# Optimization experiments

Hardware: AMD Instinct MI355X
Metric: run time of the kernel (lower is better)

The kernel has to match this reference:

```python
import jax, jax.numpy as jnp
import numpy as np

N_RAYS, N_SAMPLES = 8192, 128
RANK, RES = 32, 512


def setup_inputs() -> dict:
    key = jax.random.key(0)
    k0, k1, k2, k3 = jax.random.split(key, 4)
    pts = jax.random.uniform(k0, (N_RAYS, N_SAMPLES, 3), dtype=jnp.float32)
    # 3 plane grids for coord combos (0,1),(0,2),(1,2); torch shape [1,rank,H,W] -> [rank,H,W]
    grid_xy = jax.random.normal(k1, (RANK, RES, RES), dtype=jnp.float32) * 0.1
    grid_xz = jax.random.normal(k2, (RANK, RES, RES), dtype=jnp.float32) * 0.1
    grid_yz = jax.random.normal(k3, (RANK, RES, RES), dtype=jnp.float32) * 0.1
    aabb = jnp.array([[-1.0, -1.0, -1.0], [1.0, 1.0, 1.0]], dtype=jnp.float32)
    return {"pts": pts, "grid_xy": grid_xy, "grid_xz": grid_xz, "grid_yz": grid_yz, "aabb": aabb}


def _grid_sample2d(grid, coords):
    """Bilinear grid_sample, align_corners=True. grid [R,H,W], coords [N,2] in [-1,1] (x,y).
    Returns [N,R]."""
    H, W = grid.shape[1], grid.shape[2]
    x = (coords[:, 0] + 1.0) * 0.5 * (W - 1)
    y = (coords[:, 1] + 1.0) * 0.5 * (H - 1)
    x0 = jnp.floor(x)
    y0 = jnp.floor(y)
    wx = x - x0
    wy = y - y0
    x0i = jnp.clip(x0.astype(jnp.int32), 0, W - 1)
    x1i = jnp.clip(x0i + 1, 0, W - 1)
    y0i = jnp.clip(y0.astype(jnp.int32), 0, H - 1)
    y1i = jnp.clip(y0i + 1, 0, H - 1)
    v00 = grid[:, y0i, x0i]  # [R,N]
    v01 = grid[:, y0i, x1i]
    v10 = grid[:, y1i, x0i]
    v11 = grid[:, y1i, x1i]
    out = (v00 * (1 - wx) * (1 - wy) + v01 * wx * (1 - wy)
           + v10 * (1 - wx) * wy + v11 * wx * wy)
    return out.T  # [N,R]


def reference(pts, grid_xy, grid_xz, grid_yz, aabb):
    n_rays, n_samples, _ = pts.shape
    # normalize world coords to [-1,1]
    p = (pts - aabb[0]) * (2.0 / (aabb[1] - aabb[0])) - 1.0
    p = p.reshape(-1, 3)
    # multiply-reduce over the 3 coordinate-plane interpolations
    interp = (_grid_sample2d(grid_xy, p[:, (0, 1)])
              * _grid_sample2d(grid_xz, p[:, (0, 2)])
              * _grid_sample2d(grid_yz, p[:, (1, 2)]))  # [N, rank]
    density = jnp.mean(interp, axis=-1).reshape(n_rays, n_samples, 1)
    return jnp.exp(density)  # trunc_exp density activation
```

## Files before the change

kernel.cpp:

```cpp
#include <hip/hip_runtime.h>
#include <hip/hip_bf16.h>

#define RANK 32
#define RES  512
#define NCLS 6

typedef __attribute__((ext_vector_type(2))) float f32x2;

__device__ __forceinline__ unsigned int pack4_fp8(float a, float b, float c, float d) {
    int v = 0;
    v = __builtin_amdgcn_cvt_pk_fp8_f32(a, b, v, false);
    v = __builtin_amdgcn_cvt_pk_fp8_f32(c, d, v, true);
    return (unsigned int)v;
}

struct AxisCoord { int i0; float w; };
__device__ __forceinline__ AxisCoord axis_coord(float c) {
    float x = (c + 1.0f) * 0.5f * (float)(RES - 1);
    float fx = floorf(x);
    AxisCoord a;
    a.w  = x - fx;
    int i = (int)fx;
    a.i0 = min(max(i, 0), RES - 1);
    return a;
}

__global__ __launch_bounds__(256) void build_pairs_kernel(
    const float* __restrict__ gxy, const float* __restrict__ gxz,
    const float* __restrict__ gyz, uint4* __restrict__ pout)
{
    __shared__ __align__(16) unsigned int row[RES][RANK / 4];

    int bid   = blockIdx.x;
    int plane = bid >> 9;
    int y     = bid & (RES - 1);
    const float* g = (plane == 0) ? gxy : ((plane == 1) ? gxz : gyz);
    int t  = threadIdx.x;
    int xa = t * 2;
    const float* gr = g + (size_t)y * RES + xa;

    #pragma unroll
    for (int rq = 0; rq < RANK / 4; ++rq) {
        f32x2 f0 = *reinterpret_cast<const f32x2*>(gr + (size_t)(rq * 4 + 0) * RES * RES);
        f32x2 f1 = *reinterpret_cast<const f32x2*>(gr + (size_t)(rq * 4 + 1) * RES * RES);
        f32x2 f2 = *reinterpret_cast<const f32x2*>(gr + (size_t)(rq * 4 + 2) * RES * RES);
        f32x2 f3 = *reinterpret_cast<const f32x2*>(gr + (size_t)(rq * 4 + 3) * RES * RES);
        row[xa    ][rq] = pack4_fp8(f0.x, f1.x, f2.x, f3.x);
        row[xa + 1][rq] = pack4_fp8(f0.y, f1.y, f2.y, f3.y);
    }
    __syncthreads();

    #pragma unroll
    for (int k = 0; k < 2; ++k) {
        int x0 = t + k * 256;
        int x1 = min(x0 + 1, RES - 1);
        uint4* dst = pout + ((size_t)(plane * RES + y) * RES + x0) * 4;
        const unsigned int* r0 = row[x0];
        const unsigned int* r1 = row[x1];
        uint4 u;
        u.x = r0[0]; u.y = r0[1]; u.z = r0[2]; u.w = r0[3]; dst[0] = u;
        u.x = r0[4]; u.y = r0[5]; u.z = r0[6]; u.w = r0[7]; dst[1] = u;
        u.x = r1[0]; u.y = r1[1]; u.z = r1[2]; u.w = r1[3]; dst[2] = u;
        u.x = r1[4]; u.y = r1[5]; u.z = r1[6]; u.w = r1[7]; dst[3] = u;
    }
}

__device__ __forceinline__ void decode_plane(const uint4* __restrict__ stage,
                                             int c0, int lane,
                                             float wx, float wy,
                                             f32x2* __restrict__ v)
{
    #pragma unroll
    for (int row = 0; row < 2; ++row) {
        float rw = row ? wy : (1.0f - wy);
        float w0 = rw * (1.0f - wx);
        float w1 = rw * wx;
        #pragma unroll
        for (int jj = 0; jj < 4; ++jj) {
            uint4 q = stage[((c0 + row) * 64 + lane) * 4 + (jj ^ (lane & 3))];
            float wgt = (jj < 2) ? w0 : w1;
            int vb = (jj & 1) * 8;
            unsigned int w_[4] = { q.x, q.y, q.z, q.w };
            #pragma unroll
            for (int d = 0; d < 4; ++d) {
                f32x2 lo = __builtin_amdgcn_cvt_pk_f32_fp8((int)w_[d], false);
                f32x2 hi = __builtin_amdgcn_cvt_pk_f32_fp8((int)w_[d], true);
                int k0 = vb + d * 2, k1 = k0 + 1;
                if (row == 0 && jj < 2) {
                    v[k0].x = wgt * lo.x; v[k0].y = wgt * lo.y;
                    v[k1].x = wgt * hi.x; v[k1].y = wgt * hi.y;
                } else {
                    v[k0].x = fmaf(wgt, lo.x, v[k0].x);
                    v[k0].y = fmaf(wgt, lo.y, v[k0].y);
                    v[k1].x = fmaf(wgt, hi.x, v[k1].x);
                    v[k1].y = fmaf(wgt, hi.y, v[k1].y);
                }
            }
        }
    }
}

__global__ __launch_bounds__(64) void sample_pair_kernel(
    const float* __restrict__ pts, const unsigned char* __restrict__ table,
    const float* __restrict__ aabb, float* __restrict__ out)
{
    __shared__ __align__(16) uint4 stage[NCLS * 64 * 4];

    int lane = threadIdx.x;
    int idx  = blockIdx.x * 64 + lane;

    float px = pts[idx * 3 + 0];
    float py = pts[idx * 3 + 1];
    float pz = pts[idx * 3 + 2];

    float lox = aabb[0], loy = aabb[1], loz = aabb[2];
    float hix = aabb[3], hiy = aabb[4], hiz = aabb[5];

    float pnx = (px - lox) * (2.0f / (hix - lox)) - 1.0f;
    float pny = (py - loy) * (2.0f / (hiy - loy)) - 1.0f;
    float pnz = (pz - loz) * (2.0f / (hiz - loz)) - 1.0f;

    AxisCoord ax = axis_coord(pnx);
    AxisCoord ay = axis_coord(pny);
    AxisCoord az = axis_coord(pnz);

    int ay1 = min(ay.i0 + 1, RES - 1);
    int az1 = min(az.i0 + 1, RES - 1);

    int offs[NCLS];
    offs[0] = ((0 * RES + ay.i0) * RES + ax.i0) * 64;
    offs[1] = ((0 * RES + ay1  ) * RES + ax.i0) * 64;
    offs[2] = ((1 * RES + az.i0) * RES + ax.i0) * 64;
    offs[3] = ((1 * RES + az1  ) * RES + ax.i0) * 64;
    offs[4] = ((2 * RES + az.i0) * RES + ay.i0) * 64;
    offs[5] = ((2 * RES + az1  ) * RES + ay.i0) * 64;

    int p_this  = (lane >> 2);
    int sw_this = (lane & 3) ^ (p_this & 3);

#if __has_builtin(__builtin_amdgcn_global_load_lds)
    #pragma unroll
    for (int i = 0; i < 24; ++i) {
        const int c = i >> 2;
        const int b = i & 3;
        int p = b * 16 + p_this;
        unsigned int off = (unsigned int)__shfl(offs[c], p);
        const unsigned char* gp = table + off + sw_this * 16;
        unsigned int* lp = (unsigned int*)&stage[(c * 64 + b * 16) * 4];
        __builtin_amdgcn_global_load_lds(
            (const __attribute__((address_space(1))) unsigned int*)gp,
            (__attribute__((address_space(3))) unsigned int*)lp, 16, 0, 0);
    }
    asm volatile("s_waitcnt vmcnt(0)" ::: "memory");
    __syncthreads();
#else
    uint4 vreg[24];
    #pragma unroll
    for (int i = 0; i < 24; ++i) {
        const int c = i >> 2;
        const int b = i & 3;
        int p = b * 16 + p_this;
        unsigned int off = (unsigned int)__shfl(offs[c], p);
        vreg[i] = *reinterpret_cast<const uint4*>(table + off + sw_this * 16);
    }
    asm volatile("" ::: "memory");
    #pragma unroll
    for (int i = 0; i < 24; ++i) {
        const int c = i >> 2;
        const int b = i & 3;
        stage[(c * 64 + b * 16) * 4 + lane] = vreg[i];
    }
    __syncthreads();
#endif

    f32x2 pa[16], pb[16];
    decode_plane(stage, 0, lane, ax.w, ay.w, pa);
    decode_plane(stage, 2, lane, ax.w, az.w, pb);
    #pragma unroll
    for (int k = 0; k < 16; ++k) { pa[k].x *= pb[k].x; pa[k].y *= pb[k].y; }
    decode_plane(stage, 4, lane, ay.w, az.w, pb);

    float sx = 0.0f, sy = 0.0f;
    #pragma unroll
    for (int k = 0; k < 16; ++k) {
        sx = fmaf(pa[k].x, pb[k].x, sx);
        sy = fmaf(pa[k].y, pb[k].y, sy);
    }
    out[idx] = expf((sx + sy) * (1.0f / (float)RANK));
}

__global__ __launch_bounds__(256) void sample_direct_kernel(
    const float* __restrict__ pts,
    const float* __restrict__ gxy, const float* __restrict__ gxz,
    const float* __restrict__ gyz,
    const float* __restrict__ aabb, float* __restrict__ out, int npts)
{
    int idx = blockIdx.x * 256 + threadIdx.x;
    if (idx >= npts) return;

    float px = pts[idx * 3 + 0];
    float py = pts[idx * 3 + 1];
    float pz = pts[idx * 3 + 2];

    float lox = aabb[0], loy = aabb[1], loz = aabb[2];
    float hix = aabb[3], hiy = aabb[4], hiz = aabb[5];

    float pnx = (px - lox) * (2.0f / (hix - lox)) - 1.0f;
    float pny = (py - loy) * (2.0f / (hiy - loy)) - 1.0f;
    float pnz = (pz - loz) * (2.0f / (hiz - loz)) - 1.0f;

    AxisCoord ax = axis_coord(pnx);
    AxisCoord ay = axis_coord(pny);
    AxisCoord az = axis_coord(pnz);
    int ax1 = min(ax.i0 + 1, RES - 1);
    int ay1 = min(ay.i0 + 1, RES - 1);
    int az1 = min(az.i0 + 1, RES - 1);

    float axw = ax.w, ayw = ay.w, azw = az.w;

    int o_xy00 = ay.i0 * RES + ax.i0, o_xy01 = ay.i0 * RES + ax1;
    int o_xy10 = ay1  * RES + ax.i0, o_xy11 = ay1  * RES + ax1;
    int o_xz00 = az.i0 * RES + ax.i0, o_xz01 = az.i0 * RES + ax1;
    int o_xz10 = az1  * RES + ax.i0, o_xz11 = az1  * RES + ax1;
    int o_yz00 = az.i0 * RES + ay.i0, o_yz01 = az.i0 * RES + ay1;
    int o_yz10 = az1  * RES + ay.i0, o_yz11 = az1  * RES + ay1;

    float sum = 0.0f;
    for (int r = 0; r < RANK; ++r) {
        size_t pbs = (size_t)r * RES * RES;
        float vxy = (1-axw)*(1-ayw)*gxy[pbs+o_xy00] + axw*(1-ayw)*gxy[pbs+o_xy01]
                  + (1-axw)*ayw   *gxy[pbs+o_xy10] + axw*ayw   *gxy[pbs+o_xy11];
        float vxz = (1-axw)*(1-azw)*gxz[pbs+o_xz00] + axw*(1-azw)*gxz[pbs+o_xz01]
                  + (1-axw)*azw   *gxz[pbs+o_xz10] + axw*azw   *gxz[pbs+o_xz11];
        float vyz = (1-ayw)*(1-azw)*gyz[pbs+o_yz00] + ayw*(1-azw)*gyz[pbs+o_yz01]
                  + (1-ayw)*azw   *gyz[pbs+o_yz10] + ayw*azw   *gyz[pbs+o_yz11];
        sum += vxy * vxz * vyz;
    }
    out[idx] = expf(sum * (1.0f / (float)RANK));
}

extern "C" void kernel_launch(void* const* d_in, const int* in_sizes, int n_in,
                              void* d_out, int out_size, void* d_ws, size_t ws_size,
                              hipStream_t stream) {
    const float* pts  = (const float*)d_in[0];
    const float* gxy  = (const float*)d_in[1];
    const float* gxz  = (const float*)d_in[2];
    const float* gyz  = (const float*)d_in[3];
    const float* aabb = (const float*)d_in[4];
    float* out = (float*)d_out;

    int npts = in_sizes[0] / 3;

    size_t need_pair = (size_t)3 * RES * RES * 64;

    if (ws_size >= need_pair && (npts % 64) == 0) {
        uint4* tbl = (uint4*)d_ws;
        build_pairs_kernel<<<3 * RES, 256, 0, stream>>>(gxy, gxz, gyz, tbl);
        sample_pair_kernel<<<npts / 64, 64, 0, stream>>>(
            pts, (const unsigned char*)tbl, aabb, out);
    } else {
        int nblk = (npts + 255) / 256;
        sample_direct_kernel<<<nblk, 256, 0, stream>>>(pts, gxy, gxz, gyz, aabb, out, npts);
    }
}
```

Measured before the change: 218.7 us.

## Pack full 2x2 bilinear quads per texel and pipeline staged loads

The build kernel now stores all four bilinear corners (two rows, two columns) of FP8-packed rank vectors contiguously per texel, 128 bytes each. The sampler then issues one contiguous gather per plane instead of two row-pair gathers. The staged async loads are split with partial vmcnt waits so decoding of the first planes overlaps the remaining loads, and the block barrier is dropped. This doubles the table size, and with it the build kernel's write traffic and the workspace requirement. It also relies on each lane reading only its own LDS slots.

```diff
diff --git a/kernel.cpp b/kernel.cpp
--- a/kernel.cpp
+++ b/kernel.cpp
@@ -3,7 +3,6 @@
 
 #define RANK 32
 #define RES  512
-#define NCLS 6
 
 typedef __attribute__((ext_vector_type(2))) float f32x2;
 
@@ -25,86 +24,136 @@
     return a;
 }
 
-__global__ __launch_bounds__(256) void build_pairs_kernel(
+struct PlaneCoord {
+    int x0, y0;
+    float w00, w01, w10, w11;
+};
+
+__device__ __forceinline__ PlaneCoord make_coord(float cx, float cy) {
+    AxisCoord ax = axis_coord(cx);
+    AxisCoord ay = axis_coord(cy);
+    PlaneCoord c;
+    c.x0 = ax.i0; c.y0 = ay.i0;
+    float ix = 1.0f - ax.w, iy = 1.0f - ay.w;
+    c.w00 = ix * iy; c.w01 = ax.w * iy; c.w10 = ix * ay.w; c.w11 = ax.w * ay.w;
+    return c;
+}
+
+__global__ __launch_bounds__(256) void build_quads_kernel(
     const float* __restrict__ gxy, const float* __restrict__ gxz,
-    const float* __restrict__ gyz, uint4* __restrict__ pout)
-{
-    __shared__ __align__(16) unsigned int row[RES][RANK / 4];
+    const float* __restrict__ gyz, unsigned int* __restrict__ qout)
+{
+    __shared__ unsigned int lds[2][RES][RANK / 4];
 
     int bid   = blockIdx.x;
     int plane = bid >> 9;
-    int y     = bid & (RES - 1);
+    int y0    = bid & (RES - 1);
     const float* g = (plane == 0) ? gxy : ((plane == 1) ? gxz : gyz);
+    int y1 = min(y0 + 1, RES - 1);
     int t  = threadIdx.x;
     int xa = t * 2;
-    const float* gr = g + (size_t)y * RES + xa;
-
-    #pragma unroll
-    for (int rq = 0; rq < RANK / 4; ++rq) {
-        f32x2 f0 = *reinterpret_cast<const f32x2*>(gr + (size_t)(rq * 4 + 0) * RES * RES);
-        f32x2 f1 = *reinterpret_cast<const f32x2*>(gr + (size_t)(rq * 4 + 1) * RES * RES);
-        f32x2 f2 = *reinterpret_cast<const f32x2*>(gr + (size_t)(rq * 4 + 2) * RES * RES);
-        f32x2 f3 = *reinterpret_cast<const f32x2*>(gr + (size_t)(rq * 4 + 3) * RES * RES);
-        row[xa    ][rq] = pack4_fp8(f0.x, f1.x, f2.x, f3.x);
-        row[xa + 1][rq] = pack4_fp8(f0.y, f1.y, f2.y, f3.y);
+
+    #pragma unroll
+    for (int row = 0; row < 2; ++row) {
+        int yy = row ? y1 : y0;
+        const float* gr = g + (size_t)yy * RES + xa;
+        #pragma unroll
+        for (int rq = 0; rq < RANK / 4; ++rq) {
+            f32x2 f0 = *reinterpret_cast<const f32x2*>(gr + (size_t)(rq * 4 + 0) * RES * RES);
+            f32x2 f1 = *reinterpret_cast<const f32x2*>(gr + (size_t)(rq * 4 + 1) * RES * RES);
+            f32x2 f2 = *reinterpret_cast<const f32x2*>(gr + (size_t)(rq * 4 + 2) * RES * RES);
+            f32x2 f3 = *reinterpret_cast<const f32x2*>(gr + (size_t)(rq * 4 + 3) * RES * RES);
+            lds[row][xa    ][rq] = pack4_fp8(f0.x, f1.x, f2.x, f3.x);
+            lds[row][xa + 1][rq] = pack4_fp8(f0.y, f1.y, f2.y, f3.y);
+        }
     }
     __syncthreads();
 
     #pragma unroll
     for (int k = 0; k < 2; ++k) {
-        int x0 = t + k * 256;
-        int x1 = min(x0 + 1, RES - 1);
-        uint4* dst = pout + ((size_t)(plane * RES + y) * RES + x0) * 4;
-        const unsigned int* r0 = row[x0];
-        const unsigned int* r1 = row[x1];
+        int xr = t + k * 256;
+        int x1 = min(xr + 1, RES - 1);
+        uint4* dst = reinterpret_cast<uint4*>(qout) +
+                     ((size_t)plane * RES * RES + (size_t)y0 * RES + xr) * 8;
+        const unsigned int* t00 = lds[0][xr];
+        const unsigned int* t01 = lds[0][x1];
+        const unsigned int* t10 = lds[1][xr];
+        const unsigned int* t11 = lds[1][x1];
         uint4 u;
-        u.x = r0[0]; u.y = r0[1]; u.z = r0[2]; u.w = r0[3]; dst[0] = u;
-        u.x = r0[4]; u.y = r0[5]; u.z = r0[6]; u.w = r0[7]; dst[1] = u;
-        u.x = r1[0]; u.y = r1[1]; u.z = r1[2]; u.w = r1[3]; dst[2] = u;
-        u.x = r1[4]; u.y = r1[5]; u.z = r1[6]; u.w = r1[7]; dst[3] = u;
-    }
-}
-
-__device__ __forceinline__ void decode_plane(const uint4* __restrict__ stage,
-                                             int c0, int lane,
-                                             float wx, float wy,
-                                             f32x2* __restrict__ v)
-{
-    #pragma unroll
-    for (int row = 0; row < 2; ++row) {
-        float rw = row ? wy : (1.0f - wy);
-        float w0 = rw * (1.0f - wx);
-        float w1 = rw * wx;
+        u.x = t00[0]; u.y = t00[1]; u.z = t00[2]; u.w = t00[3]; dst[0] = u;
+        u.x = t00[4]; u.y = t00[5]; u.z = t00[6]; u.w = t00[7]; dst[1] = u;
+        u.x = t01[0]; u.y = t01[1]; u.z = t01[2]; u.w = t01[3]; dst[2] = u;
+        u.x = t01[4]; u.y = t01[5]; u.z = t01[6]; u.w = t01[7]; dst[3] = u;
+        u.x = t10[0]; u.y = t10[1]; u.z = t10[2]; u.w = t10[3]; dst[4] = u;
+        u.x = t10[4]; u.y = t10[5]; u.z = t10[6]; u.w = t10[7]; dst[5] = u;
+        u.x = t11[0]; u.y = t11[1]; u.z = t11[2]; u.w = t11[3]; dst[6] = u;
+        u.x = t11[4]; u.y = t11[5]; u.z = t11[6]; u.w = t11[7]; dst[7] = u;
+    }
+}
+
+__device__ __forceinline__ void decode_quad(const uint4* __restrict__ stage,
+                                            int c, int lane,
+                                            float w00, float w01, float w10, float w11,
+                                            f32x2* __restrict__ v)
+{
+    const float wt[4] = { w00, w01, w10, w11 };
+    #pragma unroll
+    for (int jj = 0; jj < 8; ++jj) {
+        uint4 q = stage[(c * 64 + lane) * 8 + (jj ^ (lane & 7))];
+        float wk = wt[jj >> 1];
+        int vb = (jj & 1) * 8;
+        unsigned int w_[4] = { q.x, q.y, q.z, q.w };
         #pragma unroll
-        for (int jj = 0; jj < 4; ++jj) {
-            uint4 q = stage[((c0 + row) * 64 + lane) * 4 + (jj ^ (lane & 3))];
-            float wgt = (jj < 2) ? w0 : w1;
-            int vb = (jj & 1) * 8;
-            unsigned int w_[4] = { q.x, q.y, q.z, q.w };
-            #pragma unroll
-            for (int d = 0; d < 4; ++d) {
-                f32x2 lo = __builtin_amdgcn_cvt_pk_f32_fp8((int)w_[d], false);
-                f32x2 hi = __builtin_amdgcn_cvt_pk_f32_fp8((int)w_[d], true);
-                int k0 = vb + d * 2, k1 = k0 + 1;
-                if (row == 0 && jj < 2) {
-                    v[k0].x = wgt * lo.x; v[k0].y = wgt * lo.y;
-                    v[k1].x = wgt * hi.x; v[k1].y = wgt * hi.y;
-                } else {
-                    v[k0].x = fmaf(wgt, lo.x, v[k0].x);
-                    v[k0].y = fmaf(wgt, lo.y, v[k0].y);
-                    v[k1].x = fmaf(wgt, hi.x, v[k1].x);
-                    v[k1].y = fmaf(wgt, hi.y, v[k1].y);
-                }
+        for (int d = 0; d < 4; ++d) {
+            f32x2 lo = __builtin_amdgcn_cvt_pk_f32_fp8((int)w_[d], false);
+            f32x2 hi = __builtin_amdgcn_cvt_pk_f32_fp8((int)w_[d], true);
+            int k0 = vb + d * 2, k1 = k0 + 1;
+            if (jj < 2) {
+                v[k0].x = wk * lo.x; v[k0].y = wk * lo.y;
+                v[k1].x = wk * hi.x; v[k1].y = wk * hi.y;
+            } else {
+                v[k0].x = fmaf(wk, lo.x, v[k0].x);
+                v[k0].y = fmaf(wk, lo.y, v[k0].y);
+                v[k1].x = fmaf(wk, hi.x, v[k1].x);
+                v[k1].y = fmaf(wk, hi.y, v[k1].y);
             }
         }
     }
 }
 
-__global__ __launch_bounds__(64) void sample_pair_kernel(
+__device__ __forceinline__ void decode_quad_reg(const uint4 q[8],
+                                                float w00, float w01, float w10, float w11,
+                                                f32x2* __restrict__ v)
+{
+    const float wt[4] = { w00, w01, w10, w11 };
+    #pragma unroll
+    for (int jj = 0; jj < 8; ++jj) {
+        float wk = wt[jj >> 1];
+        int vb = (jj & 1) * 8;
+        unsigned int w_[4] = { q[jj].x, q[jj].y, q[jj].z, q[jj].w };
+        #pragma unroll
+        for (int d = 0; d < 4; ++d) {
+            f32x2 lo = __builtin_amdgcn_cvt_pk_f32_fp8((int)w_[d], false);
+            f32x2 hi = __builtin_amdgcn_cvt_pk_f32_fp8((int)w_[d], true);
+            int k0 = vb + d * 2, k1 = k0 + 1;
+            if (jj < 2) {
+                v[k0].x = wk * lo.x; v[k0].y = wk * lo.y;
+                v[k1].x = wk * hi.x; v[k1].y = wk * hi.y;
+            } else {
+                v[k0].x = fmaf(wk, lo.x, v[k0].x);
+                v[k0].y = fmaf(wk, lo.y, v[k0].y);
+                v[k1].x = fmaf(wk, hi.x, v[k1].x);
+                v[k1].y = fmaf(wk, hi.y, v[k1].y);
+            }
+        }
+    }
+}
+
+__global__ __launch_bounds__(64) void sample_quad_kernel(
     const float* __restrict__ pts, const unsigned char* __restrict__ table,
     const float* __restrict__ aabb, float* __restrict__ out)
 {
-    __shared__ __align__(16) uint4 stage[NCLS * 64 * 4];
+    __shared__ __align__(16) uint4 stage[3 * 64 * 8];
 
     int lane = threadIdx.x;
     int idx  = blockIdx.x * 64 + lane;
@@ -120,65 +169,57 @@
     float pny = (py - loy) * (2.0f / (hiy - loy)) - 1.0f;
     float pnz = (pz - loz) * (2.0f / (hiz - loz)) - 1.0f;
 
-    AxisCoord ax = axis_coord(pnx);
-    AxisCoord ay = axis_coord(pny);
-    AxisCoord az = axis_coord(pnz);
-
-    int ay1 = min(ay.i0 + 1, RES - 1);
-    int az1 = min(az.i0 + 1, RES - 1);
-
-    int offs[NCLS];
-    offs[0] = ((0 * RES + ay.i0) * RES + ax.i0) * 64;
-    offs[1] = ((0 * RES + ay1  ) * RES + ax.i0) * 64;
-    offs[2] = ((1 * RES + az.i0) * RES + ax.i0) * 64;
-    offs[3] = ((1 * RES + az1  ) * RES + ax.i0) * 64;
-    offs[4] = ((2 * RES + az.i0) * RES + ay.i0) * 64;
-    offs[5] = ((2 * RES + az1  ) * RES + ay.i0) * 64;
-
-    int p_this  = (lane >> 2);
-    int sw_this = (lane & 3) ^ (p_this & 3);
+    PlaneCoord cxy = make_coord(pnx, pny);
+    PlaneCoord cxz = make_coord(pnx, pnz);
+    PlaneCoord cyz = make_coord(pny, pnz);
+
+    int offs[3];
+    offs[0] = ((0 * RES + cxy.y0) * RES + cxy.x0) * 128;
+    offs[1] = ((1 * RES + cxz.y0) * RES + cxz.x0) * 128;
+    offs[2] = ((2 * RES + cyz.y0) * RES + cyz.x0) * 128;
+
+    int p_sub = lane >> 3;
+    int sw    = (lane & 7) ^ p_sub;
 
 #if __has_builtin(__builtin_amdgcn_global_load_lds)
     #pragma unroll
     for (int i = 0; i < 24; ++i) {
-        const int c = i >> 2;
-        const int b = i & 3;
-        int p = b * 16 + p_this;
+        const int c = i >> 3;
+        const int b = i & 7;
+        int p = b * 8 + p_sub;
         unsigned int off = (unsigned int)__shfl(offs[c], p);
-        const unsigned char* gp = table + off + sw_this * 16;
-        unsigned int* lp = (unsigned int*)&stage[(c * 64 + b * 16) * 4];
+        const unsigned char* gp = table + off + sw * 16;
+        unsigned int* lp = (unsigned int*)&stage[(c * 64 + b * 8) * 8];
         __builtin_amdgcn_global_load_lds(
             (const __attribute__((address_space(1))) unsigned int*)gp,
             (__attribute__((address_space(3))) unsigned int*)lp, 16, 0, 0);
-    }
+        if ((i & 7) == 7) __builtin_amdgcn_sched_barrier(0);
+    }
+
+    f32x2 pa[16], pb[16];
+    asm volatile("s_waitcnt vmcnt(16)" ::: "memory");
+    decode_quad(stage, 0, lane, cxy.w00, cxy.w01, cxy.w10, cxy.w11, pa);
+    asm volatile("s_waitcnt vmcnt(8)" ::: "memory");
+    decode_quad(stage, 1, lane, cxz.w00, cxz.w01, cxz.w10, cxz.w11, pb);
+    #pragma unroll
+    for (int k = 0; k < 16; ++k) { pa[k].x *= pb[k].x; pa[k].y *= pb[k].y; }
     asm volatile("s_waitcnt vmcnt(0)" ::: "memory");
-    __syncthreads();
+    decode_quad(stage, 2, lane, cyz.w00, cyz.w01, cyz.w10, cyz.w11, pb);
 #else
-    uint4 vreg[24];
-    #pragma unroll
-    for (int i = 0; i < 24; ++i) {
-        const int c = i >> 2;
-        const int b = i & 3;
-        int p = b * 16 + p_this;
-        unsigned int off = (unsigned int)__shfl(offs[c], p);
-        vreg[i] = *reinterpret_cast<const uint4*>(table + off + sw_this * 16);
-    }
-    asm volatile("" ::: "memory");
-    #pragma unroll
-    for (int i = 0; i < 24; ++i) {
-        const int c = i >> 2;
-        const int b = i & 3;
-        stage[(c * 64 + b * 16) * 4 + lane] = vreg[i];
-    }
-    __syncthreads();
+    uint4 qa[8], qb[8], qc[8];
+    #pragma unroll
+    for (int i = 0; i < 8; ++i) qa[i] = *reinterpret_cast<const uint4*>(table + offs[0] + i * 16);
+    #pragma unroll
+    for (int i = 0; i < 8; ++i) qb[i] = *reinterpret_cast<const uint4*>(table + offs[1] + i * 16);
+    #pragma unroll
+    for (int i = 0; i < 8; ++i) qc[i] = *reinterpret_cast<const uint4*>(table + offs[2] + i * 16);
+    f32x2 pa[16], pb[16];
+    decode_quad_reg(qa, cxy.w00, cxy.w01, cxy.w10, cxy.w11, pa);
+    decode_quad_reg(qb, cxz.w00, cxz.w01, cxz.w10, cxz.w11, pb);
+    #pragma unroll
+    for (int k = 0; k < 16; ++k) { pa[k].x *= pb[k].x; pa[k].y *= pb[k].y; }
+    decode_quad_reg(qc, cyz.w00, cyz.w01, cyz.w10, cyz.w11, pb);
 #endif
-
-    f32x2 pa[16], pb[16];
-    decode_plane(stage, 0, lane, ax.w, ay.w, pa);
-    decode_plane(stage, 2, lane, ax.w, az.w, pb);
-    #pragma unroll
-    for (int k = 0; k < 16; ++k) { pa[k].x *= pb[k].x; pa[k].y *= pb[k].y; }
-    decode_plane(stage, 4, lane, ay.w, az.w, pb);
 
     float sx = 0.0f, sy = 0.0f;
     #pragma unroll
@@ -251,12 +292,12 @@
 
     int npts = in_sizes[0] / 3;
 
-    size_t need_pair = (size_t)3 * RES * RES * 64;
-
-    if (ws_size >= need_pair && (npts % 64) == 0) {
-        uint4* tbl = (uint4*)d_ws;
-        build_pairs_kernel<<<3 * RES, 256, 0, stream>>>(gxy, gxz, gyz, tbl);
-        sample_pair_kernel<<<npts / 64, 64, 0, stream>>>(
+    size_t need_quad = (size_t)3 * RES * RES * 128;
+
+    if (ws_size >= need_quad && (npts % 64) == 0) {
+        unsigned int* tbl = (unsigned int*)d_ws;
+        build_quads_kernel<<<3 * RES, 256, 0, stream>>>(gxy, gxz, gyz, tbl);
+        sample_quad_kernel<<<npts / 64, 64, 0, stream>>>(
             pts, (const unsigned char*)tbl, aabb, out);
     } else {
         int nblk = (npts + 255) / 256;
```

New measurement: 230.5 us. 5.4% more time.
